# Optimization experiments

Measured on AMD Instinct MI355X. Metric: run time of the kernel, lower is better.

The kernel has to match this reference:

```python
import jax, jax.numpy as jnp
import numpy as np
from jax import lax

D_MODEL = 2048
HIDDEN = 4 * D_MODEL  # SwiGLU hidden dim
CAPACITY = 0.12


def setup_inputs() -> dict:
    key = jax.random.key(0)
    ks = jax.random.split(key, 6)
    B, S, D, H = 4, 4096, D_MODEL, HIDDEN
    x = jax.random.normal(ks[0], (B, S, D), dtype=jnp.float32)
    Wr = jax.random.normal(ks[1], (D,), dtype=jnp.float32) * (1.0 / np.sqrt(D))
    Wa = jax.random.normal(ks[2], (D,), dtype=jnp.float32) * (1.0 / np.sqrt(D))
    W1 = jax.random.normal(ks[3], (D, H), dtype=jnp.float32) * (1.0 / np.sqrt(D))
    W3 = jax.random.normal(ks[4], (D, H), dtype=jnp.float32) * (1.0 / np.sqrt(D))
    W2 = jax.random.normal(ks[5], (H, D), dtype=jnp.float32) * (1.0 / np.sqrt(H))
    return {"x": x, "Wr": Wr, "Wa": Wa, "W1": W1, "W2": W2, "W3": W3}


def reference(x, Wr, Wa, W1, W2, W3):
    B, S, D = x.shape
    k = int(S * CAPACITY)  # 491

    # Router logits [B, S]
    logits = jnp.einsum('bsd,d->bs', x, Wr)

    # Top-k tokens along the sequence dim, then sort by position
    tw, ti = lax.top_k(logits, k)              # [B, k] descending weights, indices
    order = jnp.argsort(ti, axis=1)
    sel = jnp.take_along_axis(ti, order, axis=1)   # sorted token positions [B, k]
    rw = jnp.take_along_axis(tw, order, axis=1)    # weights aligned with sel [B, k]

    # Gather selected tokens [B, k, D]
    xf = jnp.take_along_axis(x, sel[..., None], axis=1)

    # SwiGLU block on the capacity-limited slice
    h = jax.nn.silu(jnp.einsum('bkd,dh->bkh', xf, W1)) * jnp.einsum('bkd,dh->bkh', xf, W3)
    y = jnp.einsum('bkh,hd->bkd', h, W2)

    # Weight by router scores and scatter-add back into the residual stream
    xw = rw[..., None] * y
    bidx = jnp.arange(B)[:, None]
    out = x.at[bidx, sel].add(xw)

    # Aux router BCE loss (x detached, as in original)
    tgt = jnp.zeros((B * S,), dtype=x.dtype).at[sel.reshape(-1)].set(1.0)
    aux_logits = jnp.einsum('nd,d->n', lax.stop_gradient(x).reshape(B * S, D), Wa)
    p = jax.nn.sigmoid(aux_logits)
    eps = 1e-7
    p = jnp.clip(p, eps, 1.0 - eps)
    aux = -jnp.mean(tgt * jnp.log(p) + (1.0 - tgt) * jnp.log1p(-p))
    return out, aux
```

## Files before the change

kernel.cpp:

```cpp
#include <hip/hip_runtime.h>

#define B_ 4
#define S_ 4096
#define D_ 2048
#define H_ 8192
#define KCAP 491
#define SLOTP 512
#define MPAD 2048

typedef __attribute__((ext_vector_type(8))) short short8;
typedef __attribute__((ext_vector_type(4))) float float4_t;

__device__ __forceinline__ unsigned short f2bf(float f) {
    unsigned int u = __float_as_uint(f);
    unsigned int r = u + 0x7fffu + ((u >> 16) & 1u);
    return (unsigned short)(r >> 16);
}

__device__ __forceinline__ void gload_lds16(const void* g, void* l) {
    __builtin_amdgcn_global_load_lds((const __attribute__((address_space(1))) void*)g,
                                     (__attribute__((address_space(3))) void*)l, 16, 0, 0);
}

__global__ __launch_bounds__(256) void k_transpose_bf16(const float* __restrict__ in,
                                                        unsigned short* __restrict__ out,
                                                        int R, int C) {
    __shared__ float s[64][65];
    int t = threadIdx.x;
    int tx = t & 15, ty = t >> 4;
    int r0 = blockIdx.x * 64, c0 = blockIdx.y * 64;
#pragma unroll
    for (int q = 0; q < 4; q++) {
        int r = ty + q * 16;
        float4 v = *(const float4*)(in + (size_t)(r0 + r) * C + c0 + tx * 4);
        s[r][tx * 4 + 0] = v.x;
        s[r][tx * 4 + 1] = v.y;
        s[r][tx * 4 + 2] = v.z;
        s[r][tx * 4 + 3] = v.w;
    }
    __syncthreads();
#pragma unroll
    for (int q = 0; q < 4; q++) {
        int c = ty + q * 16;
        ushort4 o;
        o.x = f2bf(s[tx * 4 + 0][c]);
        o.y = f2bf(s[tx * 4 + 1][c]);
        o.z = f2bf(s[tx * 4 + 2][c]);
        o.w = f2bf(s[tx * 4 + 3][c]);
        *(ushort4*)(out + (size_t)(c0 + c) * R + r0 + tx * 4) = o;
    }
}

__global__ __launch_bounds__(256) void k_router_copy(const float* __restrict__ x,
                                                     const float* __restrict__ Wr,
                                                     const float* __restrict__ Wa,
                                                     float* __restrict__ out,
                                                     float* __restrict__ logits,
                                                     float* __restrict__ auxlog) {
    int w = threadIdx.x >> 6, lane = threadIdx.x & 63;
    int row = blockIdx.x * 4 + w;
    const float* xr = x + (size_t)row * D_;
    float* orow = out + (size_t)row * D_;
    double sr = 0.0, sa = 0.0;
#pragma unroll
    for (int it = 0; it < 8; it++) {
        int off = it * 256 + lane * 4;
        float4 xv = *(const float4*)(xr + off);
        float4 rv = *(const float4*)(Wr + off);
        float4 av = *(const float4*)(Wa + off);
        *(float4*)(orow + off) = xv;
        sr += (double)xv.x * rv.x + (double)xv.y * rv.y + (double)xv.z * rv.z + (double)xv.w * rv.w;
        sa += (double)xv.x * av.x + (double)xv.y * av.y + (double)xv.z * av.z + (double)xv.w * av.w;
    }
#pragma unroll
    for (int off = 32; off > 0; off >>= 1) {
        sr += __shfl_down(sr, off);
        sa += __shfl_down(sa, off);
    }
    if (lane == 0) {
        logits[row] = (float)sr;
        auxlog[row] = (float)sa;
    }
}

__global__ __launch_bounds__(1024) void k_topk(const float* __restrict__ logits,
                                               int* __restrict__ sel, float* __restrict__ rw,
                                               int* __restrict__ flags) {
    __shared__ unsigned long long keys[S_];
    __shared__ int sarr[SLOTP];
    int b = blockIdx.x, tid = threadIdx.x;
    const float* lg = logits + (size_t)b * S_;
    for (int i = tid; i < S_; i += 1024) {
        unsigned u = __float_as_uint(lg[i]);
        u = (u & 0x80000000u) ? ~u : (u | 0x80000000u);
        keys[i] = ((unsigned long long)u << 32) | (unsigned)(S_ - 1 - i);
    }
    __syncthreads();
    for (int k = 2; k <= S_; k <<= 1) {
        for (int j = k >> 1; j > 0; j >>= 1) {
            for (int s = tid; s < S_ / 2; s += 1024) {
                int i = 2 * s - (s & (j - 1));
                int ixj = i | j;
                bool up = ((i & k) == 0);
                unsigned long long a = keys[i], c = keys[ixj];
                if ((a < c) == up) { keys[i] = c; keys[ixj] = a; }
            }
            __syncthreads();
        }
    }
    if (tid < KCAP) sarr[tid] = (int)(S_ - 1 - (unsigned)(keys[tid] & 0xFFFFFFFFull));
    __syncthreads();
    if (tid < KCAP) {
        int s = sarr[tid];
        int rank = 0;
        for (int j = 0; j < KCAP; j++) rank += (sarr[j] < s) ? 1 : 0;
        sel[b * SLOTP + rank] = s;
        rw[b * SLOTP + rank] = lg[s];
        flags[s] = 1;
    } else if (tid < SLOTP) {
        sel[b * SLOTP + tid] = 0;
        rw[b * SLOTP + tid] = 0.f;
    }
}

__global__ __launch_bounds__(256) void k_gather(const float* __restrict__ x,
                                                const int* __restrict__ sel,
                                                unsigned short* __restrict__ Abuf) {
    int row = blockIdx.x;
    int b = row >> 9, slot = row & 511;
    int tid = threadIdx.x;
    unsigned short* dst = Abuf + (size_t)row * D_ + tid * 8;
    if (slot < KCAP) {
        int tok = sel[b * SLOTP + slot];
        const float* src = x + ((size_t)(b * S_ + tok)) * D_ + tid * 8;
        float4 v0 = *(const float4*)(src);
        float4 v1 = *(const float4*)(src + 4);
        union { unsigned short us[8]; uint4 v; } pk;
        pk.us[0] = f2bf(v0.x); pk.us[1] = f2bf(v0.y); pk.us[2] = f2bf(v0.z); pk.us[3] = f2bf(v0.w);
        pk.us[4] = f2bf(v1.x); pk.us[5] = f2bf(v1.y); pk.us[6] = f2bf(v1.z); pk.us[7] = f2bf(v1.w);
        *(uint4*)dst = pk.v;
    } else {
        *(uint4*)dst = make_uint4(0u, 0u, 0u, 0u);
    }
}

__global__ __launch_bounds__(256, 3) void k_gemm1(const unsigned short* __restrict__ A,
                                                  const unsigned short* __restrict__ B1,
                                                  const unsigned short* __restrict__ B2,
                                                  unsigned short* __restrict__ Hbuf) {
    __shared__ unsigned short sA[2][128 * 32];
    __shared__ unsigned short sB1[2][64 * 32];
    __shared__ unsigned short sB2[2][64 * 32];
    const int tid = threadIdx.x;
    const int w = tid >> 6, lane = tid & 63;
    const int n0 = blockIdx.x * 64, m0 = blockIdx.y * 128;
    const int wm = (w >> 1) * 64, wn = (w & 1) * 32;
    const int srow = lane >> 2, skc = (lane & 3) * 8;
    const int lrow = lane & 15, lk = (lane >> 4) * 8;
    float4_t acc1[4][2] = {};
    float4_t acc2[4][2] = {};

    for (int k0 = 0; k0 < D_; k0 += 64) {
#pragma unroll
        for (int ks = 0; ks < 2; ks++) {
            int kk = k0 + ks * 32 + skc;
#pragma unroll
            for (int q = 0; q < 4; q++) {
                int c = w * 4 + q;
                if (c < 8) {
                    int row = c * 16 + srow;
                    gload_lds16(A + (size_t)(m0 + row) * D_ + kk, &sA[ks][c * 512]);
                } else if (c < 12) {
                    int s = c - 8, row = s * 16 + srow;
                    gload_lds16(B1 + (size_t)(n0 + row) * D_ + kk, &sB1[ks][s * 512]);
                } else {
                    int s = c - 12, row = s * 16 + srow;
                    gload_lds16(B2 + (size_t)(n0 + row) * D_ + kk, &sB2[ks][s * 512]);
                }
            }
        }
        __builtin_amdgcn_s_waitcnt(0);
        __syncthreads();
#pragma unroll
        for (int ks = 0; ks < 2; ks++) {
            short8 af[4];
#pragma unroll
            for (int i = 0; i < 4; i++)
                af[i] = *(const short8*)(&sA[ks][(wm + i * 16 + lrow) * 32 + lk]);
#pragma unroll
            for (int j = 0; j < 2; j++) {
                short8 bf1 = *(const short8*)(&sB1[ks][(wn + j * 16 + lrow) * 32 + lk]);
                short8 bf2 = *(const short8*)(&sB2[ks][(wn + j * 16 + lrow) * 32 + lk]);
#pragma unroll
                for (int i = 0; i < 4; i++) {
                    acc1[i][j] = __builtin_amdgcn_mfma_f32_16x16x32_bf16(af[i], bf1, acc1[i][j], 0, 0, 0);
                    acc2[i][j] = __builtin_amdgcn_mfma_f32_16x16x32_bf16(af[i], bf2, acc2[i][j], 0, 0, 0);
                }
            }
        }
        __syncthreads();
    }
#pragma unroll
    for (int i = 0; i < 4; i++) {
#pragma unroll
        for (int j = 0; j < 2; j++) {
            int n = n0 + wn + j * 16 + lrow;
#pragma unroll
            for (int r = 0; r < 4; r++) {
                int m = m0 + wm + i * 16 + (lane >> 4) * 4 + r;
                float g1 = acc1[i][j][r];
                float g2 = acc2[i][j][r];
                float hv = (g1 / (1.f + expf(-g1))) * g2;
                Hbuf[(size_t)m * H_ + n] = f2bf(hv);
            }
        }
    }
}

__global__ __launch_bounds__(256, 3) void k_gemm2(const unsigned short* __restrict__ A,
                                                  const unsigned short* __restrict__ Bt,
                                                  const int* __restrict__ sel,
                                                  const float* __restrict__ rw,
                                                  float* __restrict__ out) {
    __shared__ unsigned short sA[2][128 * 32];
    __shared__ unsigned short sB[2][128 * 32];
    const int tid = threadIdx.x;
    const int w = tid >> 6, lane = tid & 63;
    const int n0 = blockIdx.x * 128, m0 = blockIdx.y * 128;
    const int kbeg = blockIdx.z * (H_ / 4), kend = kbeg + H_ / 4;
    const int wm = (w >> 1) * 64, wn = (w & 1) * 64;
    const int srow = lane >> 2, skc = (lane & 3) * 8;
    const int lrow = lane & 15, lk = (lane >> 4) * 8;
    float4_t acc[4][4] = {};

    for (int k0 = kbeg; k0 < kend; k0 += 64) {
#pragma unroll
        for (int ks = 0; ks < 2; ks++) {
            int kk = k0 + ks * 32 + skc;
#pragma unroll
            for (int q = 0; q < 4; q++) {
                int c = w * 4 + q;
                int sub = c & 7;
                int row = sub * 16 + srow;
                if (c < 8)
                    gload_lds16(A + (size_t)(m0 + row) * H_ + kk, &sA[ks][sub * 512]);
                else
                    gload_lds16(Bt + (size_t)(n0 + row) * H_ + kk, &sB[ks][sub * 512]);
            }
        }
        __builtin_amdgcn_s_waitcnt(0);
        __syncthreads();
#pragma unroll
        for (int ks = 0; ks < 2; ks++) {
            short8 af[4];
#pragma unroll
            for (int i = 0; i < 4; i++)
                af[i] = *(const short8*)(&sA[ks][(wm + i * 16 + lrow) * 32 + lk]);
#pragma unroll
            for (int j = 0; j < 4; j++) {
                short8 bf = *(const short8*)(&sB[ks][(wn + j * 16 + lrow) * 32 + lk]);
#pragma unroll
                for (int i = 0; i < 4; i++)
                    acc[i][j] = __builtin_amdgcn_mfma_f32_16x16x32_bf16(af[i], bf, acc[i][j], 0, 0, 0);
            }
        }
        __syncthreads();
    }
#pragma unroll
    for (int i = 0; i < 4; i++) {
#pragma unroll
        for (int r = 0; r < 4; r++) {
            int m = m0 + wm + i * 16 + (lane >> 4) * 4 + r;
            int b = m >> 9, slot = m & 511;
            if (slot < KCAP) {
                int tok = sel[b * SLOTP + slot];
                float wgt = rw[b * SLOTP + slot];
                float* orow = out + ((size_t)(b * S_ + tok)) * D_;
#pragma unroll
                for (int j = 0; j < 4; j++) {
                    int n = n0 + wn + j * 16 + lrow;
                    atomicAdd(orow + n, wgt * acc[i][j][r]);
                }
            }
        }
    }
}

__global__ __launch_bounds__(256) void k_aux(const float* __restrict__ auxlog,
                                             const int* __restrict__ flags,
                                             float* __restrict__ auxout) {
    int i = blockIdx.x * 256 + threadIdx.x;
    float z = auxlog[i];
    float p = 1.f / (1.f + expf(-z));
    p = fminf(fmaxf(p, 1e-7f), 1.f - 1e-7f);
    int tgt = (i < S_) ? flags[i] : 0;
    float term = tgt ? logf(p) : log1pf(-p);
#pragma unroll
    for (int off = 32; off > 0; off >>= 1) term += __shfl_down(term, off);
    __shared__ float red[4];
    int w = threadIdx.x >> 6, lane = threadIdx.x & 63;
    if (lane == 0) red[w] = term;
    __syncthreads();
    if (threadIdx.x == 0) {
        float s = red[0] + red[1] + red[2] + red[3];
        atomicAdd(auxout, -s * (1.f / 16384.f));
    }
}

extern "C" void kernel_launch(void* const* d_in, const int* in_sizes, int n_in,
                              void* d_out, int out_size, void* d_ws, size_t ws_size,
                              hipStream_t stream) {
    const float* x  = (const float*)d_in[0];
    const float* Wr = (const float*)d_in[1];
    const float* Wa = (const float*)d_in[2];
    const float* W1 = (const float*)d_in[3];
    const float* W2 = (const float*)d_in[4];
    const float* W3 = (const float*)d_in[5];
    float* out = (float*)d_out;

    char* ws = (char*)d_ws;
    unsigned short* WTa  = (unsigned short*)(ws);
    unsigned short* WTb  = (unsigned short*)(ws + 33554432ull);
    unsigned short* Abuf = (unsigned short*)(ws + 67108864ull);
    unsigned short* Hbuf = (unsigned short*)(ws + 75497472ull);
    float* logits = (float*)(ws + 109051904ull);
    float* auxlog = (float*)(ws + 109117440ull);
    int*   sel    = (int*)(ws + 109182976ull);
    float* rwbuf  = (float*)(ws + 109191168ull);
    int*   flags  = (int*)(ws + 109199360ull);
    if (ws_size < 109215744ull) return;

    hipMemsetAsync(flags, 0, S_ * sizeof(int), stream);
    hipMemsetAsync(out + (size_t)B_ * S_ * D_, 0, sizeof(float), stream);

    k_transpose_bf16<<<dim3(D_ / 64, H_ / 64), 256, 0, stream>>>(W1, WTa, D_, H_);
    k_transpose_bf16<<<dim3(D_ / 64, H_ / 64), 256, 0, stream>>>(W3, WTb, D_, H_);
    k_router_copy<<<4096, 256, 0, stream>>>(x, Wr, Wa, out, logits, auxlog);
    k_topk<<<4, 1024, 0, stream>>>(logits, sel, rwbuf, flags);
    k_gather<<<MPAD, 256, 0, stream>>>(x, sel, Abuf);
    k_gemm1<<<dim3(H_ / 64, MPAD / 128), 256, 0, stream>>>(Abuf, WTa, WTb, Hbuf);
    k_transpose_bf16<<<dim3(H_ / 64, D_ / 64), 256, 0, stream>>>(W2, WTa, H_, D_);
    k_gemm2<<<dim3(D_ / 128, MPAD / 128, 4), 256, 0, stream>>>(Hbuf, WTa, sel, rwbuf, out);
    k_aux<<<64, 256, 0, stream>>>(auxlog, flags, out + (size_t)B_ * S_ * D_);
}
```

Before: 717.0 us.

## Interleave W1/W3 into one matrix and rewrite GEMMs with 256x256 triple-buffered tiles

The transpose kernel now interleaves W1 and W3 rows in 16-row groups into one combined bf16 buffer, so gemm1 runs as a single GEMM over 2H columns. Gate and up outputs land in adjacent fragments, where the SwiGLU epilogue pairs them. Both GEMMs move to 512-thread blocks with 256x256 tiles and a 3-stage LDS ring of async global-to-LDS loads with partial vmcnt waits. They also add an XOR-swizzled LDS layout against bank conflicts and raise wave priority around the MFMA blocks. The goal is more reuse per loaded byte, loads overlapped with compute, and fewer bank conflicts. The cost is heavier register pressure from 32 accumulators per wave and fewer, larger blocks.

```diff
diff --git a/kernel.cpp b/kernel.cpp
--- a/kernel.cpp
+++ b/kernel.cpp
@@ -24,7 +24,7 @@
 
 __global__ __launch_bounds__(256) void k_transpose_bf16(const float* __restrict__ in,
                                                         unsigned short* __restrict__ out,
-                                                        int R, int C) {
+                                                        int R, int C, int mode) {
     __shared__ float s[64][65];
     int t = threadIdx.x;
     int tx = t & 15, ty = t >> 4;
@@ -42,12 +42,14 @@
 #pragma unroll
     for (int q = 0; q < 4; q++) {
         int c = ty + q * 16;
+        int cg = c0 + c;
+        int orow = (mode < 0) ? cg : ((((cg >> 4) << 5) | (cg & 15)) | mode);
         ushort4 o;
         o.x = f2bf(s[tx * 4 + 0][c]);
         o.y = f2bf(s[tx * 4 + 1][c]);
         o.z = f2bf(s[tx * 4 + 2][c]);
         o.w = f2bf(s[tx * 4 + 3][c]);
-        *(ushort4*)(out + (size_t)(c0 + c) * R + r0 + tx * 4) = o;
+        *(ushort4*)(out + (size_t)orow * R + r0 + tx * 4) = o;
     }
 }
 
@@ -144,133 +146,199 @@
     }
 }
 
-__global__ __launch_bounds__(256, 3) void k_gemm1(const unsigned short* __restrict__ A,
-                                                  const unsigned short* __restrict__ B1,
-                                                  const unsigned short* __restrict__ B2,
+
+__global__ __launch_bounds__(512, 2) void k_gemm1(const unsigned short* __restrict__ A,
+                                                  const unsigned short* __restrict__ Bc,
                                                   unsigned short* __restrict__ Hbuf) {
-    __shared__ unsigned short sA[2][128 * 32];
-    __shared__ unsigned short sB1[2][64 * 32];
-    __shared__ unsigned short sB2[2][64 * 32];
+    __shared__ unsigned short lds[3 * 16384];
     const int tid = threadIdx.x;
     const int w = tid >> 6, lane = tid & 63;
-    const int n0 = blockIdx.x * 64, m0 = blockIdx.y * 128;
-    const int wm = (w >> 1) * 64, wn = (w & 1) * 32;
-    const int srow = lane >> 2, skc = (lane & 3) * 8;
-    const int lrow = lane & 15, lk = (lane >> 4) * 8;
-    float4_t acc1[4][2] = {};
-    float4_t acc2[4][2] = {};
-
-    for (int k0 = 0; k0 < D_; k0 += 64) {
-#pragma unroll
-        for (int ks = 0; ks < 2; ks++) {
-            int kk = k0 + ks * 32 + skc;
-#pragma unroll
-            for (int q = 0; q < 4; q++) {
-                int c = w * 4 + q;
-                if (c < 8) {
-                    int row = c * 16 + srow;
-                    gload_lds16(A + (size_t)(m0 + row) * D_ + kk, &sA[ks][c * 512]);
-                } else if (c < 12) {
-                    int s = c - 8, row = s * 16 + srow;
-                    gload_lds16(B1 + (size_t)(n0 + row) * D_ + kk, &sB1[ks][s * 512]);
-                } else {
-                    int s = c - 12, row = s * 16 + srow;
-                    gload_lds16(B2 + (size_t)(n0 + row) * D_ + kk, &sB2[ks][s * 512]);
-                }
+    const int wr = w >> 2, wc = w & 3;
+    const int lrow = lane & 15, l16 = lane >> 4;
+    const int w64 = tid & ~63;
+
+    int bid = blockIdx.x;
+    int m0 = (bid & 7) * 256;
+    int n0 = (bid >> 3) * 256;
+
+    const unsigned short* gA = A + (size_t)m0 * D_;
+    const unsigned short* gB = Bc + (size_t)n0 * D_;
+
+    int goff[2], dstA[2], dstB[2];
+#pragma unroll
+    for (int q = 0; q < 2; q++) {
+        int i = q * 512 + tid;
+        int row = i >> 2;
+        int slot = (i & 3) ^ ((row >> 1) & 3);
+        goff[q] = row * D_ + slot * 8;
+        dstA[q] = (q * 512 + w64) * 8;
+        dstB[q] = 8192 + (q * 512 + w64) * 8;
+    }
+
+    int offA[8], offB[4];
+#pragma unroll
+    for (int i = 0; i < 8; i++) {
+        int r = wr * 128 + i * 16 + lrow;
+        offA[i] = r * 32 + (l16 ^ ((r >> 1) & 3)) * 8;
+    }
+#pragma unroll
+    for (int j = 0; j < 4; j++) {
+        int r = wc * 64 + j * 16 + lrow;
+        offB[j] = 8192 + r * 32 + (l16 ^ ((r >> 1) & 3)) * 8;
+    }
+
+    float4_t acc[8][4] = {};
+
+#define STAGE1(buf, kt)                                       \
+    {                                                         \
+        unsigned short* sb_ = lds + (buf) * 16384;            \
+        gload_lds16(gA + goff[0] + (kt), sb_ + dstA[0]);      \
+        gload_lds16(gA + goff[1] + (kt), sb_ + dstA[1]);      \
+        gload_lds16(gB + goff[0] + (kt), sb_ + dstB[0]);      \
+        gload_lds16(gB + goff[1] + (kt), sb_ + dstB[1]);      \
+    }
+
+    STAGE1(0, 0);
+    STAGE1(1, 32);
+    asm volatile("s_waitcnt vmcnt(4)" ::: "memory");
+    __builtin_amdgcn_s_barrier();
+
+    const int NT = D_ / 32;
+    int cur = 0, nx = 2;
+    for (int t = 0; t < NT; t++) {
+        if (t + 2 < NT) STAGE1(nx, (t + 2) * 32);
+        const unsigned short* sb = lds + cur * 16384;
+        short8 af[8], bf[4];
+#pragma unroll
+        for (int i = 0; i < 8; i++) af[i] = *(const short8*)(sb + offA[i]);
+#pragma unroll
+        for (int j = 0; j < 4; j++) bf[j] = *(const short8*)(sb + offB[j]);
+        __builtin_amdgcn_s_setprio(1);
+#pragma unroll
+        for (int j = 0; j < 4; j++)
+#pragma unroll
+            for (int i = 0; i < 8; i++)
+                acc[i][j] = __builtin_amdgcn_mfma_f32_16x16x32_bf16(af[i], bf[j], acc[i][j], 0, 0, 0);
+        __builtin_amdgcn_s_setprio(0);
+        if (t + 1 < NT) {
+            __builtin_amdgcn_sched_barrier(0);
+            if (t + 2 < NT) asm volatile("s_waitcnt vmcnt(4)" ::: "memory");
+            else            asm volatile("s_waitcnt vmcnt(0)" ::: "memory");
+            __builtin_amdgcn_s_barrier();
+        }
+        cur = (cur == 2) ? 0 : cur + 1;
+        nx  = (nx == 2) ? 0 : nx + 1;
+    }
+#undef STAGE1
+
+#pragma unroll
+    for (int i = 0; i < 8; i++) {
+        int mbase = m0 + wr * 128 + i * 16 + l16 * 4;
+#pragma unroll
+        for (int jp = 0; jp < 2; jp++) {
+            int np = n0 + wc * 64 + jp * 32 + lrow;
+            int col = ((np >> 5) << 4) | (np & 15);
+#pragma unroll
+            for (int r = 0; r < 4; r++) {
+                float g1 = acc[i][2 * jp][r];
+                float g2 = acc[i][2 * jp + 1][r];
+                float hv = (g1 / (1.f + expf(-g1))) * g2;
+                Hbuf[(size_t)(mbase + r) * H_ + col] = f2bf(hv);
             }
         }
-        __builtin_amdgcn_s_waitcnt(0);
-        __syncthreads();
-#pragma unroll
-        for (int ks = 0; ks < 2; ks++) {
-            short8 af[4];
-#pragma unroll
-            for (int i = 0; i < 4; i++)
-                af[i] = *(const short8*)(&sA[ks][(wm + i * 16 + lrow) * 32 + lk]);
-#pragma unroll
-            for (int j = 0; j < 2; j++) {
-                short8 bf1 = *(const short8*)(&sB1[ks][(wn + j * 16 + lrow) * 32 + lk]);
-                short8 bf2 = *(const short8*)(&sB2[ks][(wn + j * 16 + lrow) * 32 + lk]);
-#pragma unroll
-                for (int i = 0; i < 4; i++) {
-                    acc1[i][j] = __builtin_amdgcn_mfma_f32_16x16x32_bf16(af[i], bf1, acc1[i][j], 0, 0, 0);
-                    acc2[i][j] = __builtin_amdgcn_mfma_f32_16x16x32_bf16(af[i], bf2, acc2[i][j], 0, 0, 0);
-                }
-            }
-        }
-        __syncthreads();
-    }
-#pragma unroll
-    for (int i = 0; i < 4; i++) {
-#pragma unroll
-        for (int j = 0; j < 2; j++) {
-            int n = n0 + wn + j * 16 + lrow;
-#pragma unroll
-            for (int r = 0; r < 4; r++) {
-                int m = m0 + wm + i * 16 + (lane >> 4) * 4 + r;
-                float g1 = acc1[i][j][r];
-                float g2 = acc2[i][j][r];
-                float hv = (g1 / (1.f + expf(-g1))) * g2;
-                Hbuf[(size_t)m * H_ + n] = f2bf(hv);
-            }
-        }
-    }
-}
-
-__global__ __launch_bounds__(256, 3) void k_gemm2(const unsigned short* __restrict__ A,
+    }
+}
+
+__global__ __launch_bounds__(512, 2) void k_gemm2(const unsigned short* __restrict__ A,
                                                   const unsigned short* __restrict__ Bt,
                                                   const int* __restrict__ sel,
                                                   const float* __restrict__ rw,
                                                   float* __restrict__ out) {
-    __shared__ unsigned short sA[2][128 * 32];
-    __shared__ unsigned short sB[2][128 * 32];
+    __shared__ unsigned short lds[3 * 16384];
     const int tid = threadIdx.x;
     const int w = tid >> 6, lane = tid & 63;
-    const int n0 = blockIdx.x * 128, m0 = blockIdx.y * 128;
-    const int kbeg = blockIdx.z * (H_ / 4), kend = kbeg + H_ / 4;
-    const int wm = (w >> 1) * 64, wn = (w & 1) * 64;
-    const int srow = lane >> 2, skc = (lane & 3) * 8;
-    const int lrow = lane & 15, lk = (lane >> 4) * 8;
-    float4_t acc[4][4] = {};
-
-    for (int k0 = kbeg; k0 < kend; k0 += 64) {
-#pragma unroll
-        for (int ks = 0; ks < 2; ks++) {
-            int kk = k0 + ks * 32 + skc;
-#pragma unroll
-            for (int q = 0; q < 4; q++) {
-                int c = w * 4 + q;
-                int sub = c & 7;
-                int row = sub * 16 + srow;
-                if (c < 8)
-                    gload_lds16(A + (size_t)(m0 + row) * H_ + kk, &sA[ks][sub * 512]);
-                else
-                    gload_lds16(Bt + (size_t)(n0 + row) * H_ + kk, &sB[ks][sub * 512]);
-            }
+    const int wr = w >> 2, wc = w & 3;
+    const int lrow = lane & 15, l16 = lane >> 4;
+    const int w64 = tid & ~63;
+
+    const int n0 = blockIdx.x * 256, m0 = blockIdx.y * 256;
+    const int kbeg = blockIdx.z * (H_ / 4);
+
+    const unsigned short* gA = A + (size_t)m0 * H_ + kbeg;
+    const unsigned short* gB = Bt + (size_t)n0 * H_ + kbeg;
+
+    int goff[2], dstA[2], dstB[2];
+#pragma unroll
+    for (int q = 0; q < 2; q++) {
+        int i = q * 512 + tid;
+        int row = i >> 2;
+        int slot = (i & 3) ^ ((row >> 1) & 3);
+        goff[q] = row * H_ + slot * 8;
+        dstA[q] = (q * 512 + w64) * 8;
+        dstB[q] = 8192 + (q * 512 + w64) * 8;
+    }
+
+    int offA[8], offB[4];
+#pragma unroll
+    for (int i = 0; i < 8; i++) {
+        int r = wr * 128 + i * 16 + lrow;
+        offA[i] = r * 32 + (l16 ^ ((r >> 1) & 3)) * 8;
+    }
+#pragma unroll
+    for (int j = 0; j < 4; j++) {
+        int r = wc * 64 + j * 16 + lrow;
+        offB[j] = 8192 + r * 32 + (l16 ^ ((r >> 1) & 3)) * 8;
+    }
+
+    float4_t acc[8][4] = {};
+
+#define STAGE2(buf, kt)                                       \
+    {                                                         \
+        unsigned short* sb_ = lds + (buf) * 16384;            \
+        gload_lds16(gA + goff[0] + (kt), sb_ + dstA[0]);      \
+        gload_lds16(gA + goff[1] + (kt), sb_ + dstA[1]);      \
+        gload_lds16(gB + goff[0] + (kt), sb_ + dstB[0]);      \
+        gload_lds16(gB + goff[1] + (kt), sb_ + dstB[1]);      \
+    }
+
+    STAGE2(0, 0);
+    STAGE2(1, 32);
+    asm volatile("s_waitcnt vmcnt(4)" ::: "memory");
+    __builtin_amdgcn_s_barrier();
+
+    const int NT = (H_ / 4) / 32;
+    int cur = 0, nx = 2;
+    for (int t = 0; t < NT; t++) {
+        if (t + 2 < NT) STAGE2(nx, (t + 2) * 32);
+        const unsigned short* sb = lds + cur * 16384;
+        short8 af[8], bf[4];
+#pragma unroll
+        for (int i = 0; i < 8; i++) af[i] = *(const short8*)(sb + offA[i]);
+#pragma unroll
+        for (int j = 0; j < 4; j++) bf[j] = *(const short8*)(sb + offB[j]);
+        __builtin_amdgcn_s_setprio(1);
+#pragma unroll
+        for (int j = 0; j < 4; j++)
+#pragma unroll
+            for (int i = 0; i < 8; i++)
+                acc[i][j] = __builtin_amdgcn_mfma_f32_16x16x32_bf16(af[i], bf[j], acc[i][j], 0, 0, 0);
+        __builtin_amdgcn_s_setprio(0);
+        if (t + 1 < NT) {
+            __builtin_amdgcn_sched_barrier(0);
+            if (t + 2 < NT) asm volatile("s_waitcnt vmcnt(4)" ::: "memory");
+            else            asm volatile("s_waitcnt vmcnt(0)" ::: "memory");
+            __builtin_amdgcn_s_barrier();
         }
-        __builtin_amdgcn_s_waitcnt(0);
-        __syncthreads();
-#pragma unroll
-        for (int ks = 0; ks < 2; ks++) {
-            short8 af[4];
-#pragma unroll
-            for (int i = 0; i < 4; i++)
-                af[i] = *(const short8*)(&sA[ks][(wm + i * 16 + lrow) * 32 + lk]);
-#pragma unroll
-            for (int j = 0; j < 4; j++) {
-                short8 bf = *(const short8*)(&sB[ks][(wn + j * 16 + lrow) * 32 + lk]);
-#pragma unroll
-                for (int i = 0; i < 4; i++)
-                    acc[i][j] = __builtin_amdgcn_mfma_f32_16x16x32_bf16(af[i], bf, acc[i][j], 0, 0, 0);
-            }
-        }
-        __syncthreads();
-    }
-#pragma unroll
-    for (int i = 0; i < 4; i++) {
+        cur = (cur == 2) ? 0 : cur + 1;
+        nx  = (nx == 2) ? 0 : nx + 1;
+    }
+#undef STAGE2
+
+#pragma unroll
+    for (int i = 0; i < 8; i++) {
 #pragma unroll
         for (int r = 0; r < 4; r++) {
-            int m = m0 + wm + i * 16 + (lane >> 4) * 4 + r;
+            int m = m0 + wr * 128 + i * 16 + l16 * 4 + r;
             int b = m >> 9, slot = m & 511;
             if (slot < KCAP) {
                 int tok = sel[b * SLOTP + slot];
@@ -278,7 +346,7 @@
                 float* orow = out + ((size_t)(b * S_ + tok)) * D_;
 #pragma unroll
                 for (int j = 0; j < 4; j++) {
-                    int n = n0 + wn + j * 16 + lrow;
+                    int n = n0 + wc * 64 + j * 16 + lrow;
                     atomicAdd(orow + n, wgt * acc[i][j][r]);
                 }
             }
@@ -319,8 +387,7 @@
     float* out = (float*)d_out;
 
     char* ws = (char*)d_ws;
-    unsigned short* WTa  = (unsigned short*)(ws);
-    unsigned short* WTb  = (unsigned short*)(ws + 33554432ull);
+    unsigned short* WTc  = (unsigned short*)(ws);
     unsigned short* Abuf = (unsigned short*)(ws + 67108864ull);
     unsigned short* Hbuf = (unsigned short*)(ws + 75497472ull);
     float* logits = (float*)(ws + 109051904ull);
@@ -333,13 +400,13 @@
     hipMemsetAsync(flags, 0, S_ * sizeof(int), stream);
     hipMemsetAsync(out + (size_t)B_ * S_ * D_, 0, sizeof(float), stream);
 
-    k_transpose_bf16<<<dim3(D_ / 64, H_ / 64), 256, 0, stream>>>(W1, WTa, D_, H_);
-    k_transpose_bf16<<<dim3(D_ / 64, H_ / 64), 256, 0, stream>>>(W3, WTb, D_, H_);
+    k_transpose_bf16<<<dim3(D_ / 64, H_ / 64), 256, 0, stream>>>(W1, WTc, D_, H_, 0);
+    k_transpose_bf16<<<dim3(D_ / 64, H_ / 64), 256, 0, stream>>>(W3, WTc, D_, H_, 16);
     k_router_copy<<<4096, 256, 0, stream>>>(x, Wr, Wa, out, logits, auxlog);
     k_topk<<<4, 1024, 0, stream>>>(logits, sel, rwbuf, flags);
     k_gather<<<MPAD, 256, 0, stream>>>(x, sel, Abuf);
-    k_gemm1<<<dim3(H_ / 64, MPAD / 128), 256, 0, stream>>>(Abuf, WTa, WTb, Hbuf);
-    k_transpose_bf16<<<dim3(H_ / 64, D_ / 64), 256, 0, stream>>>(W2, WTa, H_, D_);
-    k_gemm2<<<dim3(D_ / 128, MPAD / 128, 4), 256, 0, stream>>>(Hbuf, WTa, sel, rwbuf, out);
+    k_gemm1<<<512, 512, 0, stream>>>(Abuf, WTc, Hbuf);
+    k_transpose_bf16<<<dim3(H_ / 64, D_ / 64), 256, 0, stream>>>(W2, WTc, H_, D_, -1);
+    k_gemm2<<<dim3(D_ / 256, MPAD / 256, 4), 512, 0, stream>>>(Hbuf, WTc, sel, rwbuf, out);
     k_aux<<<64, 256, 0, stream>>>(auxlog, flags, out + (size_t)B_ * S_ * D_);
 }
```

After: 679.4 us. -5.2%, faster.
